# Kernel optimization log

Measured on AMD Instinct MI355X. Metric: run time of the kernel, lower is better.

Reference implementation:

```python
import jax, jax.numpy as jnp
import numpy as np

FL = 320       # frame length
FS = 80        # frame shift
ORDER = 16     # poly order (a[0] == 1)
EMPH = 0.97    # pre/de-emphasis coefficient


def setup_inputs() -> dict:
    key = jax.random.key(0)
    k1, k2 = jax.random.split(key)
    B, F = 64, 3000
    L = F * FS  # 240000
    excit = jax.random.normal(k1, (B, L, 1), dtype=jnp.float32) * 0.1
    # LPC coefficients: a[0] = 1, remaining taps small for numerical stability
    rest = jax.random.normal(k2, (B, F, ORDER - 1), dtype=jnp.float32) * (0.3 / (ORDER - 1))
    lpc_coef = jnp.concatenate([jnp.ones((B, F, 1), jnp.float32), rest], axis=-1)
    return {"excit": excit, "lpc_coef": lpc_coef}


def reference(excit, lpc_coef):
    """LPCSynthesisPytorch: AR synthesis recursion followed by de-emphasis.

    excit:    (B, L, 1)
    lpc_coef: (B, F, order), a[0] assumed 1, L = F * FS
    returns:  (B, L, 1)
    """
    B, L, _ = excit.shape
    order = lpc_coef.shape[-1]

    # Per-sample AR taps a[1:], expanded frame->sample, time-major for scan.
    a = jnp.repeat(lpc_coef[:, :, 1:], FS, axis=1)[:, :L]      # (B, L, order-1)
    a_t = jnp.transpose(a, (1, 0, 2))                          # (L, B, order-1)
    e_t = jnp.transpose(excit[..., 0], (1, 0))                 # (L, B)

    def ar_step(buf, inp):
        # buf: (B, order-1) = [x[n-order+1], ..., x[n-1]] (last entry most recent)
        a_n, e_n = inp
        # predicted = sum_k a[k] * x[n-k]; output = excit - predicted
        pre = -jnp.sum(a_n * buf[:, ::-1], axis=-1)
        out = e_n + pre
        buf = jnp.concatenate([buf[:, 1:], out[:, None]], axis=-1)
        return buf, out

    buf0 = jnp.zeros((B, order - 1), dtype=excit.dtype)
    _, y_t = jax.lax.scan(ar_step, buf0, (a_t, e_t))           # (L, B)

    # De-emphasis IIR: z[n] = y[n] + EMPH * z[n-1], z[-1] = 0
    def deemph_step(prev, x):
        cur = x + EMPH * prev
        return cur, cur

    _, z_t = jax.lax.scan(deemph_step, jnp.zeros((B,), excit.dtype), y_t)
    return jnp.transpose(z_t, (1, 0))[..., None]               # (B, L, 1)
```

## Files before the change

kernel.cpp:

```cpp
#include <hip/hip_runtime.h>


namespace {
constexpr int kFS = 80;
constexpr int kF = 3000;
constexpr int kL = kFS * kF;
constexpr int kOrder = 16;
constexpr int kB = 64;
constexpr float kEmph = 0.97f;
constexpr int kThreads = 128;
constexpr int kEmit = kThreads - 4;
constexpr int kSE = 84;
constexpr float kR1 = 0.08744575f;
constexpr float kR2 = 0.00764676f;
constexpr float kR3 = 6.6872537e-4f;
constexpr float kLg97 = -4.3943347e-2f;

typedef float vfloat4 __attribute__((ext_vector_type(4)));
typedef _Float16 half4v __attribute__((ext_vector_type(4)));
}

__global__ __launch_bounds__(kThreads) void lpc_synth_kernel(
    const float* __restrict__ excit, const float* __restrict__ coef,
    float* __restrict__ out) {
  __shared__ _Float16 s_e[kThreads * kSE];
  __shared__ float s_zend[kThreads];

  const int tid = threadIdx.x;
  const int b = blockIdx.y;
  const int fbase = blockIdx.x * kEmit;
  const int Lf = fbase - 4 + tid;
  const int Lc = min(max(Lf, 0), kF - 1);
  const int Lw = min(max(Lf - 1, 0), kF - 1);

  const float* __restrict__ ebase = excit + (size_t)b * kL;
  const float* __restrict__ cbase = coef + (size_t)b * kF * kOrder;

  const vfloat4* __restrict__ cw =
      (const vfloat4*)(cbase + (size_t)Lw * kOrder);
  const vfloat4* __restrict__ ce =
      (const vfloat4*)(cbase + (size_t)Lc * kOrder);
  const vfloat4 w0 = cw[0], w1 = cw[1], w2 = cw[2], w3 = cw[3];
  const vfloat4 e0 = ce[0], e1 = ce[1], e2 = ce[2], e3 = ce[3];

  {
    const vfloat4* __restrict__ ep =
        (const vfloat4*)(ebase + (size_t)Lc * kFS);
    half4v* se = (half4v*)(s_e + tid * kSE);
#pragma unroll
    for (int j = 0; j < 20; ++j) {
      const vfloat4 v = ep[j];
      half4v h;
      h.x = (_Float16)v.x;
      h.y = (_Float16)v.y;
      h.z = (_Float16)v.z;
      h.w = (_Float16)v.w;
      se[j] = h;
    }
  }
  __syncthreads();

  float x[16];
#pragma unroll
  for (int i = 0; i < 16; ++i) x[i] = 0.f;

#define AR_SAMPLE(s, e_in, ACC)                                            \
  float ACC;                                                               \
  {                                                                        \
    float a0 = (e_in);                                                     \
    a0 = fmaf(-a_[14], x[((s)-15) & 15], a0);                              \
    a0 = fmaf(-a_[13], x[((s)-14) & 15], a0);                              \
    a0 = fmaf(-a_[12], x[((s)-13) & 15], a0);                              \
    a0 = fmaf(-a_[11], x[((s)-12) & 15], a0);                              \
    a0 = fmaf(-a_[10], x[((s)-11) & 15], a0);                              \
    float a1 = -a_[9] * x[((s)-10) & 15];                                  \
    a1 = fmaf(-a_[8], x[((s)-9) & 15], a1);                                \
    a1 = fmaf(-a_[7], x[((s)-8) & 15], a1);                                \
    a1 = fmaf(-a_[6], x[((s)-7) & 15], a1);                                \
    a1 = fmaf(-a_[5], x[((s)-6) & 15], a1);                                \
    float a2 = -a_[4] * x[((s)-5) & 15];                                   \
    a2 = fmaf(-a_[3], x[((s)-4) & 15], a2);                                \
    a2 = fmaf(-a_[2], x[((s)-3) & 15], a2);                                \
    a2 = fmaf(-a_[1], x[((s)-2) & 15], a2);                                \
    const float a01 = a0 + a1;                      \
    a2 = fmaf(-a_[0], x[((s)-1) & 15], a2);           \
    ACC = a01 + a2;                                           \
    x[(s)&15] = ACC;                                                       \
  }

  {
    const int wslot = max(tid - 1, 0);
    const half4v* __restrict__ ses = (const half4v*)(s_e + wslot * kSE);
    const float a_[15] = {w0.y, w0.z, w0.w, w1.x, w1.y, w1.z, w1.w,
                          w2.x, w2.y, w2.z, w2.w, w3.x, w3.y, w3.z, w3.w};
#pragma unroll
    for (int j = 8; j < 20; ++j) {
      const half4v h = ses[j];
      const float f_[4] = {(float)h.x, (float)h.y, (float)h.z, (float)h.w};
#pragma unroll
      for (int q = 0; q < 4; ++q) {
        AR_SAMPLE(4 * j + q, f_[q], acc)
        (void)acc;
      }
    }
  }
  if (Lf <= 0) {
#pragma unroll
    for (int i = 0; i < 16; ++i) x[i] = 0.f;
  }
  float z = 0.f;
  __syncthreads();

  {
    half4v* __restrict__ ses = (half4v*)(s_e + tid * kSE);
    const float a_[15] = {e0.y, e0.z, e0.w, e1.x, e1.y, e1.z, e1.w,
                          e2.x, e2.y, e2.z, e2.w, e3.x, e3.y, e3.z, e3.w};
#pragma unroll
    for (int j = 0; j < 20; ++j) {
      const half4v h = ses[j];
      const float f_[4] = {(float)h.x, (float)h.y, (float)h.z, (float)h.w};
      half4v ho;
#pragma unroll
      for (int q = 0; q < 4; ++q) {
        AR_SAMPLE(4 * j + q, f_[q], acc)
        z = fmaf(kEmph, z, acc);
        if (q == 0) ho.x = (_Float16)z;
        if (q == 1) ho.y = (_Float16)z;
        if (q == 2) ho.z = (_Float16)z;
        if (q == 3) ho.w = (_Float16)z;
      }
      ses[j] = ho;
    }
  }
#undef AR_SAMPLE
  s_zend[tid] = (Lf < 0 || Lf >= kF) ? 0.f : z;
  __syncthreads();

  {
    const int nfr = min(kEmit, kF - fbase);
    const int nv4 = nfr * 20;
    vfloat4* __restrict__ ob =
        (vfloat4*)(out + (size_t)b * kL + (size_t)fbase * kFS);
#pragma unroll 1
    for (int i = tid; i < nv4; i += kThreads) {
      const int k = i / 20;
      const int j = i % 20;
      const half4v h = *(const half4v*)(s_e + (k + 4) * kSE + 4 * j);
      float Zp = s_zend[k + 3];
      Zp = fmaf(kR1, s_zend[k + 2], Zp);
      Zp = fmaf(kR2, s_zend[k + 1], Zp);
      Zp = fmaf(kR3, s_zend[k], Zp);
      const float ee = __builtin_exp2f(kLg97 * (float)(4 * j + 1));
      vfloat4 v;
      v.x = fmaf(ee, Zp, (float)h.x);
      v.y = fmaf(ee * 0.97f, Zp, (float)h.y);
      v.z = fmaf(ee * 0.9409f, Zp, (float)h.z);
      v.w = fmaf(ee * 0.912673f, Zp, (float)h.w);
      ob[i] = v;
    }
  }
}

extern "C" void kernel_launch(void* const* d_in, const int* in_sizes, int n_in,
                              void* d_out, int out_size, void* d_ws,
                              size_t ws_size, hipStream_t stream) {
  const float* excit = (const float*)d_in[0];
  const float* coef = (const float*)d_in[1];
  float* out = (float*)d_out;

  dim3 grid((kF + kEmit - 1) / kEmit, kB);
  lpc_synth_kernel<<<grid, kThreads, 0, stream>>>(excit, coef, out);
}
```

Baseline: 126.9 us.

## Split frames into half-frame chunks per thread with longer warmup

```diff
diff --git a/kernel.cpp b/kernel.cpp
--- a/kernel.cpp
+++ b/kernel.cpp
@@ -3,18 +3,26 @@
 
 namespace {
 constexpr int kFS = 80;
+constexpr int kHS = 40;
 constexpr int kF = 3000;
+constexpr int kH = 2 * kF;
 constexpr int kL = kFS * kF;
 constexpr int kOrder = 16;
 constexpr int kB = 64;
 constexpr float kEmph = 0.97f;
 constexpr int kThreads = 128;
-constexpr int kEmit = kThreads - 4;
-constexpr int kSE = 84;
-constexpr float kR1 = 0.08744575f;
-constexpr float kR2 = 0.00764676f;
-constexpr float kR3 = 6.6872537e-4f;
+constexpr int kJunk = 9;
+constexpr int kEmitH = kThreads - kJunk;
+constexpr int kSEH = 44;
 constexpr float kLg97 = -4.3943347e-2f;
+constexpr float kR1 = 0.2957118f;
+constexpr float kR2 = 0.08744547f;
+constexpr float kR3 = 0.02585867f;
+constexpr float kR4 = 0.00764671f;
+constexpr float kR5 = 0.00226126f;
+constexpr float kR6 = 6.6867e-4f;
+constexpr float kR7 = 1.9773e-4f;
+constexpr float kR8 = 5.8472e-5f;
 
 typedef float vfloat4 __attribute__((ext_vector_type(4)));
 typedef _Float16 half4v __attribute__((ext_vector_type(4)));
@@ -23,32 +31,35 @@
 __global__ __launch_bounds__(kThreads) void lpc_synth_kernel(
     const float* __restrict__ excit, const float* __restrict__ coef,
     float* __restrict__ out) {
-  __shared__ _Float16 s_e[kThreads * kSE];
+  __shared__ _Float16 s_e[kThreads * kSEH];
   __shared__ float s_zend[kThreads];
+  __shared__ float s_zp[kThreads];
 
   const int tid = threadIdx.x;
   const int b = blockIdx.y;
-  const int fbase = blockIdx.x * kEmit;
-  const int Lf = fbase - 4 + tid;
-  const int Lc = min(max(Lf, 0), kF - 1);
-  const int Lw = min(max(Lf - 1, 0), kF - 1);
+  const int hbase = blockIdx.x * kEmitH;
+  const int ht = hbase + tid - kJunk;
+  const int hc = min(max(ht, 0), kH - 1);
+  const int hw = min(max(ht - 2, 0), kH - 1);
 
   const float* __restrict__ ebase = excit + (size_t)b * kL;
   const float* __restrict__ cbase = coef + (size_t)b * kF * kOrder;
 
-  const vfloat4* __restrict__ cw =
-      (const vfloat4*)(cbase + (size_t)Lw * kOrder);
-  const vfloat4* __restrict__ ce =
-      (const vfloat4*)(cbase + (size_t)Lc * kOrder);
-  const vfloat4 w0 = cw[0], w1 = cw[1], w2 = cw[2], w3 = cw[3];
-  const vfloat4 e0 = ce[0], e1 = ce[1], e2 = ce[2], e3 = ce[3];
+  const int fprev = hw >> 1;
+  const int fcur = hc >> 1;
+  const vfloat4* __restrict__ cp =
+      (const vfloat4*)(cbase + (size_t)fprev * kOrder);
+  const vfloat4* __restrict__ cc =
+      (const vfloat4*)(cbase + (size_t)fcur * kOrder);
+  const vfloat4 p0 = cp[0], p1 = cp[1], p2 = cp[2], p3 = cp[3];
+  const vfloat4 q0 = cc[0], q1 = cc[1], q2 = cc[2], q3 = cc[3];
 
   {
     const vfloat4* __restrict__ ep =
-        (const vfloat4*)(ebase + (size_t)Lc * kFS);
-    half4v* se = (half4v*)(s_e + tid * kSE);
-#pragma unroll
-    for (int j = 0; j < 20; ++j) {
+        (const vfloat4*)(ebase + (size_t)hc * kHS);
+    half4v* se = (half4v*)(s_e + tid * kSEH);
+#pragma unroll
+    for (int j = 0; j < 10; ++j) {
       const vfloat4 v = ep[j];
       half4v h;
       h.x = (_Float16)v.x;
@@ -64,65 +75,83 @@
 #pragma unroll
   for (int i = 0; i < 16; ++i) x[i] = 0.f;
 
-#define AR_SAMPLE(s, e_in, ACC)                                            \
+  float pa_[15] = {p0.y, p0.z, p0.w, p1.x, p1.y, p1.z, p1.w,
+                   p2.x, p2.y, p2.z, p2.w, p3.x, p3.y, p3.z, p3.w};
+  const float ca_[15] = {q0.y, q0.z, q0.w, q1.x, q1.y, q1.z, q1.w,
+                         q2.x, q2.y, q2.z, q2.w, q3.x, q3.y, q3.z, q3.w};
+
+#define AR_SAMPLE(A, s, e_in, ACC)                                         \
   float ACC;                                                               \
   {                                                                        \
-    float a0 = (e_in);                                                     \
-    a0 = fmaf(-a_[14], x[((s)-15) & 15], a0);                              \
-    a0 = fmaf(-a_[13], x[((s)-14) & 15], a0);                              \
-    a0 = fmaf(-a_[12], x[((s)-13) & 15], a0);                              \
-    a0 = fmaf(-a_[11], x[((s)-12) & 15], a0);                              \
-    a0 = fmaf(-a_[10], x[((s)-11) & 15], a0);                              \
-    float a1 = -a_[9] * x[((s)-10) & 15];                                  \
-    a1 = fmaf(-a_[8], x[((s)-9) & 15], a1);                                \
-    a1 = fmaf(-a_[7], x[((s)-8) & 15], a1);                                \
-    a1 = fmaf(-a_[6], x[((s)-7) & 15], a1);                                \
-    a1 = fmaf(-a_[5], x[((s)-6) & 15], a1);                                \
-    float a2 = -a_[4] * x[((s)-5) & 15];                                   \
-    a2 = fmaf(-a_[3], x[((s)-4) & 15], a2);                                \
-    a2 = fmaf(-a_[2], x[((s)-3) & 15], a2);                                \
-    a2 = fmaf(-a_[1], x[((s)-2) & 15], a2);                                \
-    const float a01 = a0 + a1;                      \
-    a2 = fmaf(-a_[0], x[((s)-1) & 15], a2);           \
-    ACC = a01 + a2;                                           \
+    float t0 = (e_in);                                                     \
+    t0 = fmaf(-A[14], x[((s)-15) & 15], t0);                               \
+    t0 = fmaf(-A[13], x[((s)-14) & 15], t0);                               \
+    t0 = fmaf(-A[12], x[((s)-13) & 15], t0);                               \
+    t0 = fmaf(-A[11], x[((s)-12) & 15], t0);                               \
+    t0 = fmaf(-A[10], x[((s)-11) & 15], t0);                               \
+    float t1 = -A[9] * x[((s)-10) & 15];                                   \
+    t1 = fmaf(-A[8], x[((s)-9) & 15], t1);                                 \
+    t1 = fmaf(-A[7], x[((s)-8) & 15], t1);                                 \
+    t1 = fmaf(-A[6], x[((s)-7) & 15], t1);                                 \
+    t1 = fmaf(-A[5], x[((s)-6) & 15], t1);                                 \
+    float t2 = -A[4] * x[((s)-5) & 15];                                    \
+    t2 = fmaf(-A[3], x[((s)-4) & 15], t2);                                 \
+    t2 = fmaf(-A[2], x[((s)-3) & 15], t2);                                 \
+    t2 = fmaf(-A[1], x[((s)-2) & 15], t2);                                 \
+    const float t01 = t0 + t1;                      \
+    t2 = fmaf(-A[0], x[((s)-1) & 15], t2);            \
+    ACC = t01 + t2;                                           \
     x[(s)&15] = ACC;                                                       \
   }
 
   {
-    const int wslot = max(tid - 1, 0);
-    const half4v* __restrict__ ses = (const half4v*)(s_e + wslot * kSE);
-    const float a_[15] = {w0.y, w0.z, w0.w, w1.x, w1.y, w1.z, w1.w,
-                          w2.x, w2.y, w2.z, w2.w, w3.x, w3.y, w3.z, w3.w};
-#pragma unroll
-    for (int j = 8; j < 20; ++j) {
-      const half4v h = ses[j];
-      const float f_[4] = {(float)h.x, (float)h.y, (float)h.z, (float)h.w};
+    const half4v* __restrict__ s2 =
+        (const half4v*)(s_e + max(tid - 2, 0) * kSEH);
+    const half4v* __restrict__ s1 =
+        (const half4v*)(s_e + max(tid - 1, 0) * kSEH);
+    const float m2 = (ht >= 2) ? 1.f : 0.f;
+    const float m1 = (ht >= 1) ? 1.f : 0.f;
+#pragma unroll
+    for (int j = 0; j < 2; ++j) {
+      const half4v h = s2[8 + j];
+      const float f_[4] = {m2 * (float)h.x, m2 * (float)h.y,
+                           m2 * (float)h.z, m2 * (float)h.w};
 #pragma unroll
       for (int q = 0; q < 4; ++q) {
-        AR_SAMPLE(4 * j + q, f_[q], acc)
+        AR_SAMPLE(pa_, 4 * j + q, f_[q], acc)
         (void)acc;
       }
     }
-  }
-  if (Lf <= 0) {
-#pragma unroll
-    for (int i = 0; i < 16; ++i) x[i] = 0.f;
-  }
+    if (ht & 1) {
+#pragma unroll
+      for (int k = 0; k < 15; ++k) pa_[k] = ca_[k];
+    }
+#pragma unroll
+    for (int j = 0; j < 10; ++j) {
+      const half4v h = s1[j];
+      const float f_[4] = {m1 * (float)h.x, m1 * (float)h.y,
+                           m1 * (float)h.z, m1 * (float)h.w};
+#pragma unroll
+      for (int q = 0; q < 4; ++q) {
+        AR_SAMPLE(pa_, 8 + 4 * j + q, f_[q], acc)
+        (void)acc;
+      }
+    }
+  }
+
   float z = 0.f;
   __syncthreads();
 
   {
-    half4v* __restrict__ ses = (half4v*)(s_e + tid * kSE);
-    const float a_[15] = {e0.y, e0.z, e0.w, e1.x, e1.y, e1.z, e1.w,
-                          e2.x, e2.y, e2.z, e2.w, e3.x, e3.y, e3.z, e3.w};
-#pragma unroll
-    for (int j = 0; j < 20; ++j) {
+    half4v* __restrict__ ses = (half4v*)(s_e + tid * kSEH);
+#pragma unroll
+    for (int j = 0; j < 10; ++j) {
       const half4v h = ses[j];
       const float f_[4] = {(float)h.x, (float)h.y, (float)h.z, (float)h.w};
       half4v ho;
 #pragma unroll
       for (int q = 0; q < 4; ++q) {
-        AR_SAMPLE(4 * j + q, f_[q], acc)
+        AR_SAMPLE(ca_, 48 + 4 * j + q, f_[q], acc)
         z = fmaf(kEmph, z, acc);
         if (q == 0) ho.x = (_Float16)z;
         if (q == 1) ho.y = (_Float16)z;
@@ -133,23 +162,34 @@
     }
   }
 #undef AR_SAMPLE
-  s_zend[tid] = (Lf < 0 || Lf >= kF) ? 0.f : z;
-  __syncthreads();
-
-  {
-    const int nfr = min(kEmit, kF - fbase);
-    const int nv4 = nfr * 20;
+  s_zend[tid] = (ht < 0 || ht >= kH) ? 0.f : z;
+  __syncthreads();
+
+  if (tid < kEmitH) {
+    float Zp = s_zend[tid + 8];
+    Zp = fmaf(kR1, s_zend[tid + 7], Zp);
+    Zp = fmaf(kR2, s_zend[tid + 6], Zp);
+    Zp = fmaf(kR3, s_zend[tid + 5], Zp);
+    Zp = fmaf(kR4, s_zend[tid + 4], Zp);
+    Zp = fmaf(kR5, s_zend[tid + 3], Zp);
+    Zp = fmaf(kR6, s_zend[tid + 2], Zp);
+    Zp = fmaf(kR7, s_zend[tid + 1], Zp);
+    Zp = fmaf(kR8, s_zend[tid + 0], Zp);
+    s_zp[tid] = Zp;
+  }
+  __syncthreads();
+
+  {
+    const int nfr = min(kEmitH, kH - hbase);
+    const int nv4 = nfr * 10;
     vfloat4* __restrict__ ob =
-        (vfloat4*)(out + (size_t)b * kL + (size_t)fbase * kFS);
+        (vfloat4*)(out + (size_t)b * kL + (size_t)hbase * kHS);
 #pragma unroll 1
     for (int i = tid; i < nv4; i += kThreads) {
-      const int k = i / 20;
-      const int j = i % 20;
-      const half4v h = *(const half4v*)(s_e + (k + 4) * kSE + 4 * j);
-      float Zp = s_zend[k + 3];
-      Zp = fmaf(kR1, s_zend[k + 2], Zp);
-      Zp = fmaf(kR2, s_zend[k + 1], Zp);
-      Zp = fmaf(kR3, s_zend[k], Zp);
+      const int k = i / 10;
+      const int j = i % 10;
+      const half4v h = *(const half4v*)(s_e + (k + kJunk) * kSEH + 4 * j);
+      const float Zp = s_zp[k];
       const float ee = __builtin_exp2f(kLg97 * (float)(4 * j + 1));
       vfloat4 v;
       v.x = fmaf(ee, Zp, (float)h.x);
@@ -168,6 +208,6 @@
   const float* coef = (const float*)d_in[1];
   float* out = (float*)d_out;
 
-  dim3 grid((kF + kEmit - 1) / kEmit, kB);
+  dim3 grid((kH + kEmitH - 1) / kEmitH, kB);
   lpc_synth_kernel<<<grid, kThreads, 0, stream>>>(excit, coef, out);
 }
```

Measured after the change: 124.8 us. About the same (-1.6%).
